# Kernel optimization log

Measured on AMD Instinct MI355X. Metric: run time of the kernel, lower is better.

## Reference

```python
import jax, jax.numpy as jnp
import numpy as np

N_NODES = 50000
N_EDGES = 800000
N_GRAPHS = 2500
HIDDEN = 64
IN_DIM = 14  # 11 QM9 features + 3 pos


def setup_inputs() -> dict:
    key = jax.random.key(0)
    ks = jax.random.split(key, 12)
    def glorot(k, shape):
        fan_in = shape[0]
        return jax.random.normal(k, shape, dtype=jnp.float32) / np.sqrt(fan_in)
    return {
        "x": jax.random.normal(ks[0], (N_NODES, 11), dtype=jnp.float32),
        "pos": jax.random.normal(ks[1], (N_NODES, 3), dtype=jnp.float32),
        "edge_index": jax.random.randint(ks[2], (2, N_EDGES), 0, N_NODES, dtype=jnp.int64),
        "batch": jnp.sort(jax.random.randint(ks[3], (N_NODES,), 0, N_GRAPHS, dtype=jnp.int64)),
        "W1a": glorot(ks[4], (IN_DIM, HIDDEN)),
        "b1a": jnp.zeros((HIDDEN,), jnp.float32),
        "W1b": glorot(ks[5], (HIDDEN, HIDDEN)),
        "b1b": jnp.zeros((HIDDEN,), jnp.float32),
        "W2a": glorot(ks[6], (HIDDEN, HIDDEN)),
        "b2a": jnp.zeros((HIDDEN,), jnp.float32),
        "W2b": glorot(ks[7], (HIDDEN, HIDDEN)),
        "b2b": jnp.zeros((HIDDEN,), jnp.float32),
        "Wlin": glorot(ks[8], (HIDDEN, 1)),
        "blin": jnp.zeros((1,), jnp.float32),
    }


def reference(x, pos, edge_index, batch, W1a, b1a, W1b, b1b, W2a, b2a, W2b, b2b, Wlin, blin):
    n = x.shape[0]
    src, dst = edge_index[0], edge_index[1]

    def gin_conv(h, Wa, ba, Wb, bb):
        # GINConv (eps=0): nn((1+eps)*h + sum_{j in N(i)} h_j)
        agg = jax.ops.segment_sum(h[src], dst, num_segments=n)  # scatter-add over edges
        z = h + agg
        return jax.nn.relu(z @ Wa + ba) @ Wb + bb

    h = jnp.concatenate([x, pos], axis=1)  # [N, 14]
    h = jax.nn.relu(gin_conv(h, W1a, b1a, W1b, b1b))
    h = jax.nn.relu(gin_conv(h, W2a, b2a, W2b, b2b))

    # global_mean_pool over graph ids
    sums = jax.ops.segment_sum(h, batch, num_segments=N_GRAPHS)            # [G, H]
    counts = jax.ops.segment_sum(jnp.ones((n,), h.dtype), batch, num_segments=N_GRAPHS)
    pooled = sums / jnp.maximum(counts, 1.0)[:, None]
    return pooled @ Wlin + blin  # [G, 1]
```

## Files before the change

kernel.cpp:

```cpp
#include <hip/hip_runtime.h>
#include <hip/hip_fp16.h>


typedef unsigned int uint;
typedef _Float16 half8 __attribute__((ext_vector_type(8)));
typedef float f32x4 __attribute__((ext_vector_type(4)));

#define BSH   6
#define NBKMAX 1024
#define EPB   4096
#define CAPSH 11
#define CAP   (1 << CAPSH)
#define ZBLK  64

__device__ __forceinline__ void addu(float* a, uint d) {
    __half2 h = *(__half2*)&d;
    a[0] += __low2float(h);
    a[1] += __high2float(h);
}
__device__ __forceinline__ half8 as_half8(uint4 u) {
    union { uint4 u; half8 h; } x; x.u = u; return x.h;
}


__global__ __launch_bounds__(256) void pack_bin(
    const float* __restrict__ x, const float* __restrict__ pos,
    uint2* __restrict__ xp2,
    const int* __restrict__ src, const int* __restrict__ dst,
    int* __restrict__ bkt_cnt, uint* __restrict__ pairs,
    const float* __restrict__ W1a, const float* __restrict__ W1b,
    const float* __restrict__ W2a, const float* __restrict__ W2b,
    _Float16* __restrict__ wp1a, _Float16* __restrict__ wp1b,
    _Float16* __restrict__ wp2a, _Float16* __restrict__ wp2b,
    uint4* __restrict__ zbuf, int nz4,
    int packb, int nbk, int N, int E)
{
    int bx = (int)blockIdx.x;
    if (bx < ZBLK) {
        uint4 z4 = {0u, 0u, 0u, 0u};
        for (int idx = bx * 256 + threadIdx.x; idx < nz4; idx += ZBLK * 256)
            zbuf[idx] = z4;
        return;
    }
    bx -= ZBLK;
    if (bx == 0) {
        for (int idx = threadIdx.x; idx < 64 * 32; idx += 256) {
            int n = idx >> 5, k = idx & 31;
            wp1a[idx] = (k < 14) ? (_Float16)W1a[k * 64 + n] : (_Float16)0.f;
        }
        for (int idx = threadIdx.x; idx < 64 * 64; idx += 256) {
            int n = idx >> 6, k = idx & 63;
            wp1b[idx] = (_Float16)W1b[k * 64 + n];
            wp2a[idx] = (_Float16)W2a[k * 64 + n];
            wp2b[idx] = (_Float16)W2b[k * 64 + n];
        }
        return;
    }
    bx -= 1;
    if (bx < packb) {
        int i = bx * 256 + threadIdx.x;
        if (i >= N) return;
        float v[16];
#pragma unroll
        for (int k = 0; k < 11; k++) v[k] = x[(size_t)i * 11 + k];
        v[11] = pos[(size_t)i * 3 + 0];
        v[12] = pos[(size_t)i * 3 + 1];
        v[13] = pos[(size_t)i * 3 + 2];
        v[14] = 0.f; v[15] = 0.f;
#pragma unroll
        for (int c = 0; c < 4; c++) {
            __half2 l = __floats2half2_rn(v[4 * c],     v[4 * c + 1]);
            __half2 h = __floats2half2_rn(v[4 * c + 2], v[4 * c + 3]);
            uint2 u;
            u.x = *(uint*)&l;
            u.y = *(uint*)&h;
            xp2[(size_t)i * 4 + c] = u;
        }
        return;
    }
    bx -= packb;
    __shared__ int lcnt[NBKMAX];
    __shared__ int lbase[NBKMAX];
    int tid = threadIdx.x;
    for (int i = tid; i < nbk; i += 256) lcnt[i] = 0;
    __syncthreads();
    int eb = bx * EPB;
    uint pv[16];
    int  rk[16], bk[16];
    if (eb + EPB <= E) {
        const int4* s4 = (const int4*)(src + eb) + tid * 4;
        const int4* d4 = (const int4*)(dst + eb) + tid * 4;
        int4 sv[4], dv[4];
#pragma unroll
        for (int g = 0; g < 4; g++) { sv[g] = s4[g]; dv[g] = d4[g]; }
#pragma unroll
        for (int g = 0; g < 4; g++) {
            int ss[4] = {sv[g].x, sv[g].y, sv[g].z, sv[g].w};
            int dd[4] = {dv[g].x, dv[g].y, dv[g].z, dv[g].w};
#pragma unroll
            for (int k = 0; k < 4; k++) {
                int j = g * 4 + k;
                bk[j] = dd[k] >> BSH;
                pv[j] = ((uint)(dd[k] & ((1 << BSH) - 1)) << 16) | (uint)ss[k];
            }
        }
#pragma unroll
        for (int j = 0; j < 16; j++)
            rk[j] = atomicAdd(&lcnt[bk[j]], 1);
    } else {
#pragma unroll
        for (int j = 0; j < 16; j++) {
            int e = eb + tid * 16 + j;
            bk[j] = -1;
            if (e < E) {
                int s = src[e];
                int d = dst[e];
                bk[j] = d >> BSH;
                pv[j] = ((uint)(d & ((1 << BSH) - 1)) << 16) | (uint)s;
            }
        }
#pragma unroll
        for (int j = 0; j < 16; j++)
            if (bk[j] >= 0) rk[j] = atomicAdd(&lcnt[bk[j]], 1);
    }
    __syncthreads();
    for (int i = tid; i < nbk; i += 256) {
        int c = lcnt[i];
        lbase[i] = c ? atomicAdd(&bkt_cnt[i], c) : 0;
    }
    __syncthreads();
#pragma unroll
    for (int j = 0; j < 16; j++) {
        if (bk[j] >= 0) {
            int p = lbase[bk[j]] + rk[j];
            if (p < CAP)
                pairs[((size_t)bk[j] << CAPSH) + p] = pv[j];
        }
    }
}


__global__ __launch_bounds__(256) void bucket_build(
    const uint* __restrict__ pairs, const int* __restrict__ bkt_cnt,
    int* __restrict__ offs, int* __restrict__ deg,
    int* __restrict__ ssrc, int N)
{
    __shared__ int cnt[64];
    __shared__ int cur[64];
    int b = blockIdx.x;
    int nbase = b << BSH;
    int nn = min(1 << BSH, N - nbase);
    int tid = threadIdx.x;
    if (tid < 64) cnt[tid] = 0;
    __syncthreads();
    int start = b << CAPSH;
    int cntE = min(bkt_cnt[b], CAP);
    uint pr[8];
#pragma unroll
    for (int k = 0; k < 8; k++) {
        int e = tid + k * 256;
        pr[k] = (e < cntE) ? pairs[start + e] : 0xffffffffu;
    }
#pragma unroll
    for (int k = 0; k < 8; k++)
        if (pr[k] != 0xffffffffu) atomicAdd(&cnt[pr[k] >> 16], 1);
    __syncthreads();
    if (tid < 64) {
        int v = cnt[tid];
        int s = v;
#pragma unroll
        for (int o2 = 1; o2 < 64; o2 <<= 1) {
            int t = __shfl_up(s, o2, 64);
            if (tid >= o2) s += t;
        }
        int gofs = start + s - v;
        if (tid < nn) {
            offs[nbase + tid] = gofs;
            deg[nbase + tid]  = v;
        }
        cur[tid] = gofs;
    }
    __syncthreads();
#pragma unroll
    for (int k = 0; k < 8; k++)
        if (pr[k] != 0xffffffffu) {
            int p = atomicAdd(&cur[pr[k] >> 16], 1);
            ssrc[p] = (int)(pr[k] & 0xffffu);
        }
}


__global__ __launch_bounds__(256) void gather1_mlp1(
    const uint2* __restrict__ xp2,
    const int* __restrict__ offs, const int* __restrict__ deg,
    const int* __restrict__ ssrc,
    const _Float16* __restrict__ wp1a, const _Float16* __restrict__ wp1b,
    const float* __restrict__ b1a, const float* __restrict__ b1b,
    uint* __restrict__ h1p)
{
    __shared__ uint4 zb[16 * 2];
    __shared__ float hb[16 * 68];
    int lane = threadIdx.x & 63;
    int wid  = threadIdx.x >> 6;
    int i0 = blockIdx.x << 4;
    int n0 = i0 + wid * 4;

    int stv = 0, lnv = 0;
    if (lane < 4) { stv = offs[n0 + lane]; lnv = deg[n0 + lane]; }
    int n  = lane >> 4;
    int s  = (lane >> 2) & 3;
    int c  = lane & 3;
    int dn = __shfl(lnv, n, 64);
    int st = __shfl(stv, n, 64);
    int pA = lane & 15;
    int svA = 0, svB = 0;
    if (dn > 0)  svA = ssrc[st + min(pA, dn - 1)];
    if (dn > 16) svB = ssrc[st + min(16 + pA, dn - 1)];
    uint2 S = {0u, 0u};
    if (s == 0) S = xp2[(size_t)(n0 + n) * 4 + c];

    float a[4] = {0.f, 0.f, 0.f, 0.f};
#pragma unroll
    for (int it = 0; it < 4; ++it) {
        int pos = it * 4 + s;
        int sA = __shfl(svA, (n << 4) | pos, 64);
        if (pos < dn) {
            uint2 A = xp2[(size_t)sA * 4 + c];
            addu(a + 0, A.x); addu(a + 2, A.y);
        }
    }
    if (__any(dn > 16)) {
#pragma unroll
        for (int it = 4; it < 8; ++it) {
            int pos = it * 4 + s;
            int sB = __shfl(svB, (n << 4) | (pos - 16), 64);
            if (pos < dn) {
                uint2 A = xp2[(size_t)sB * 4 + c];
                addu(a + 0, A.x); addu(a + 2, A.y);
            }
        }
        int pos2 = 32 + s;
        while (__any(pos2 < dn)) {
            if (pos2 < dn) {
                int sid = ssrc[st + pos2];
                uint2 A = xp2[(size_t)sid * 4 + c];
                addu(a + 0, A.x); addu(a + 2, A.y);
            }
            pos2 += 4;
        }
    }
#pragma unroll
    for (int mm = 4; mm <= 8; mm <<= 1)
#pragma unroll
        for (int d = 0; d < 4; d++) a[d] += __shfl_xor(a[d], mm, 64);
    if (s == 0) {
        addu(a + 0, S.x); addu(a + 2, S.y);
        __half2 l  = __floats2half2_rn(a[0], a[1]);
        __half2 hh = __floats2half2_rn(a[2], a[3]);
        uint2 u;
        u.x = *(uint*)&l;
        u.y = *(uint*)&hh;
        ((uint2*)zb)[(wid * 4 + n) * 4 + c] = u;
    }
    __syncthreads();

    int m = lane & 15, quad = lane >> 4;
    int half = lane >> 5, p = lane & 31;
    int nw = wid * 16 + m;
    half8 BA  = *(const half8*)(wp1a + (size_t)nw * 32 + quad * 8);
    half8 BB0 = *(const half8*)(wp1b + (size_t)nw * 64 + quad * 8);
    half8 BB1 = *(const half8*)(wp1b + (size_t)nw * 64 + 32 + quad * 8);
    float baw = b1a[nw], bbw = b1b[nw];

    half8 A0;
#pragma unroll
    for (int jj = 0; jj < 8; jj++) A0[jj] = (_Float16)0.f;
    if (quad < 2)
        A0 = as_half8(zb[m * 2 + quad]);
    f32x4 acc = (f32x4){baw, baw, baw, baw};
    acc = __builtin_amdgcn_mfma_f32_16x16x32_f16(A0, BA, acc, 0, 0, 0);
#pragma unroll
    for (int r = 0; r < 4; r++)
        hb[(quad * 4 + r) * 68 + wid * 16 + m] = fmaxf(acc[r], 0.f);
    __syncthreads();
    half8 A1[2];
#pragma unroll
    for (int hh = 0; hh < 2; hh++)
#pragma unroll
        for (int jj = 0; jj < 8; jj++)
            A1[hh][jj] = (_Float16)hb[m * 68 + hh * 32 + quad * 8 + jj];
    f32x4 acc2 = (f32x4){bbw, bbw, bbw, bbw};
    acc2 = __builtin_amdgcn_mfma_f32_16x16x32_f16(A1[0], BB0, acc2, 0, 0, 0);
    acc2 = __builtin_amdgcn_mfma_f32_16x16x32_f16(A1[1], BB1, acc2, 0, 0, 0);
    __syncthreads();
#pragma unroll
    for (int r = 0; r < 4; r++)
        hb[(quad * 4 + r) * 68 + wid * 16 + m] = fmaxf(acc2[r], 0.f);
    __syncthreads();
#pragma unroll
    for (int it = 0; it < 2; it++) {
        int row = wid * 4 + it * 2 + half;
        float lo = hb[row * 68 + 2 * p];
        float hi = hb[row * 68 + 2 * p + 1];
        __half2 hh2 = __floats2half2_rn(lo, hi);
        h1p[(size_t)(i0 + row) * 32 + p] = *(uint*)&hh2;
    }
}


__global__ __launch_bounds__(256) void gather2_mlp2pool(
    const uint4* __restrict__ h4,
    const int* __restrict__ offs, const int* __restrict__ deg,
    const int* __restrict__ ssrc,
    const _Float16* __restrict__ wp2a, const _Float16* __restrict__ wp2b,
    const float* __restrict__ b2a, const float* __restrict__ b2b,
    const int* __restrict__ batch,
    float* __restrict__ sums, float* __restrict__ counts)
{
    __shared__ uint4 zb[16 * 8];
    __shared__ float hb[16 * 68];
    int lane = threadIdx.x & 63;
    int wid  = threadIdx.x >> 6;
    int i0 = blockIdx.x << 4;
    int n0 = i0 + wid * 4;

    int stv = 0, lnv = 0;
    if (lane < 4) { stv = offs[n0 + lane]; lnv = deg[n0 + lane]; }
    int n  = lane >> 4;
    int s  = (lane >> 3) & 1;
    int q  = lane & 7;
    int dn = __shfl(lnv, n, 64);
    int st = __shfl(stv, n, 64);
    int pA = lane & 15;
    int svA = 0, svB = 0;
    if (dn > 0)  svA = ssrc[st + min(pA, dn - 1)];
    if (dn > 16) svB = ssrc[st + min(16 + pA, dn - 1)];
    uint4 S = {0u, 0u, 0u, 0u};
    if (s == 0) S = h4[(size_t)(n0 + n) * 8 + q];

    float a[8] = {0.f, 0.f, 0.f, 0.f, 0.f, 0.f, 0.f, 0.f};
#pragma unroll
    for (int it = 0; it < 8; ++it) {
        int pos = it * 2 + s;
        int sA = __shfl(svA, (n << 4) | pos, 64);
        if (pos < dn) {
            uint4 A = h4[(size_t)sA * 8 + q];
            addu(a + 0, A.x); addu(a + 2, A.y); addu(a + 4, A.z); addu(a + 6, A.w);
        }
    }
    if (__any(dn > 16)) {
#pragma unroll
        for (int it = 8; it < 16; ++it) {
            int pos = it * 2 + s;
            int sB = __shfl(svB, (n << 4) | (pos - 16), 64);
            if (pos < dn) {
                uint4 A = h4[(size_t)sB * 8 + q];
                addu(a + 0, A.x); addu(a + 2, A.y); addu(a + 4, A.z); addu(a + 6, A.w);
            }
        }
        int pos2 = 32 + s;
        while (__any(pos2 < dn)) {
            if (pos2 < dn) {
                int sid = ssrc[st + pos2];
                uint4 A = h4[(size_t)sid * 8 + q];
                addu(a + 0, A.x); addu(a + 2, A.y); addu(a + 4, A.z); addu(a + 6, A.w);
            }
            pos2 += 2;
        }
    }
#pragma unroll
    for (int d = 0; d < 8; d++) a[d] += __shfl_xor(a[d], 8, 64);
    if (s == 0) {
        addu(a + 0, S.x); addu(a + 2, S.y); addu(a + 4, S.z); addu(a + 6, S.w);
        __half2 p0 = __floats2half2_rn(a[0], a[1]);
        __half2 p1 = __floats2half2_rn(a[2], a[3]);
        __half2 p2 = __floats2half2_rn(a[4], a[5]);
        __half2 p3 = __floats2half2_rn(a[6], a[7]);
        uint4 o4;
        o4.x = *(uint*)&p0; o4.y = *(uint*)&p1;
        o4.z = *(uint*)&p2; o4.w = *(uint*)&p3;
        zb[(wid * 4 + n) * 8 + q] = o4;
    }
    __syncthreads();

    int m = lane & 15, quad = lane >> 4;
    int nw = wid * 16 + m;
    half8 BA0 = *(const half8*)(wp2a + (size_t)nw * 64 + quad * 8);
    half8 BA1 = *(const half8*)(wp2a + (size_t)nw * 64 + 32 + quad * 8);
    half8 BB0 = *(const half8*)(wp2b + (size_t)nw * 64 + quad * 8);
    half8 BB1 = *(const half8*)(wp2b + (size_t)nw * 64 + 32 + quad * 8);
    float baw = b2a[nw], bbw = b2b[nw];

    half8 A0[2];
#pragma unroll
    for (int hh = 0; hh < 2; hh++)
        A0[hh] = as_half8(zb[m * 8 + hh * 4 + quad]);
    f32x4 acc = (f32x4){baw, baw, baw, baw};
    acc = __builtin_amdgcn_mfma_f32_16x16x32_f16(A0[0], BA0, acc, 0, 0, 0);
    acc = __builtin_amdgcn_mfma_f32_16x16x32_f16(A0[1], BA1, acc, 0, 0, 0);
#pragma unroll
    for (int r = 0; r < 4; r++)
        hb[(quad * 4 + r) * 68 + wid * 16 + m] = fmaxf(acc[r], 0.f);
    __syncthreads();
    half8 A1[2];
#pragma unroll
    for (int hh = 0; hh < 2; hh++)
#pragma unroll
        for (int jj = 0; jj < 8; jj++)
            A1[hh][jj] = (_Float16)hb[m * 68 + hh * 32 + quad * 8 + jj];
    f32x4 acc2 = (f32x4){bbw, bbw, bbw, bbw};
    acc2 = __builtin_amdgcn_mfma_f32_16x16x32_f16(A1[0], BB0, acc2, 0, 0, 0);
    acc2 = __builtin_amdgcn_mfma_f32_16x16x32_f16(A1[1], BB1, acc2, 0, 0, 0);
    __syncthreads();
#pragma unroll
    for (int r = 0; r < 4; r++)
        hb[(quad * 4 + r) * 68 + wid * 16 + m] = fmaxf(acc2[r], 0.f);
    __syncthreads();

    int gcur = batch[i0 + wid * 4]; float ps = 0.f; int cntn = 0;
#pragma unroll
    for (int nn = 0; nn < 4; nn++) {
        int row = wid * 4 + nn;
        float v = hb[row * 68 + lane];
        int gi = batch[i0 + row];
        if (gi != gcur) {
            atomicAdd(&sums[gcur * 64 + lane], ps);
            if (lane == 0) atomicAdd(&counts[gcur], (float)cntn);
            gcur = gi; ps = 0.f; cntn = 0;
        }
        ps += v; cntn++;
    }
    atomicAdd(&sums[gcur * 64 + lane], ps);
    if (lane == 0) atomicAdd(&counts[gcur], (float)cntn);
}

__global__ __launch_bounds__(256) void gin_final(
    const float* __restrict__ sums, const float* __restrict__ counts,
    const float* __restrict__ Wlin, const float* __restrict__ blin,
    float* __restrict__ out, int G)
{
    int lane = threadIdx.x & 63;
    int g    = blockIdx.x * 4 + (threadIdx.x >> 6);
    if (g < G) {
        float v = sums[g * 64 + lane] * Wlin[lane];
#pragma unroll
        for (int off = 32; off > 0; off >>= 1) v += __shfl_down(v, off, 64);
        if (lane == 0) out[g] = v / fmaxf(counts[g], 1.0f) + blin[0];
    }
}

extern "C" void kernel_launch(void* const* d_in, const int* in_sizes, int n_in,
                              void* d_out, int out_size, void* d_ws, size_t ws_size,
                              hipStream_t stream) {
    const float* x    = (const float*)d_in[0];
    const float* pos  = (const float*)d_in[1];
    const int*   ei   = (const int*)d_in[2];
    const int*   batch= (const int*)d_in[3];
    const float* W1a  = (const float*)d_in[4];
    const float* b1a  = (const float*)d_in[5];
    const float* W1b  = (const float*)d_in[6];
    const float* b1b  = (const float*)d_in[7];
    const float* W2a  = (const float*)d_in[8];
    const float* b2a  = (const float*)d_in[9];
    const float* W2b  = (const float*)d_in[10];
    const float* b2b  = (const float*)d_in[11];
    const float* Wlin = (const float*)d_in[12];
    const float* blin = (const float*)d_in[13];
    float* out = (float*)d_out;

    const int N = in_sizes[0] / 11;
    const int E = in_sizes[2] / 2;
    const int G = out_size;

    const int* src = ei;
    const int* dst = ei + E;
    const int nbk   = (N + (1 << BSH) - 1) >> BSH;
    const int packb = (N + 255) / 256;
    const int neb   = (E + EPB - 1) / EPB;
    const int NG    = N >> 4;

    char* ws = (char*)d_ws;
    size_t o = 0;
    float* sums    = (float*)(ws + o); o += (size_t)G * 64 * 4;
    float* counts  = (float*)(ws + o); o += (((size_t)G + 63) & ~(size_t)63) * 4;
    const int nz4  = (int)(((size_t)G * 64 + (((size_t)G + 63) & ~(size_t)63)) / 4);
    int*   bkt_cnt = (int*)(ws + o);   o += NBKMAX * 4;
    o = (o + 255) & ~(size_t)255;
    _Float16* wp1a = (_Float16*)(ws + o); o += 64 * 32 * 2;
    o = (o + 255) & ~(size_t)255;
    _Float16* wp1b = (_Float16*)(ws + o); o += 64 * 64 * 2;
    o = (o + 255) & ~(size_t)255;
    _Float16* wp2a = (_Float16*)(ws + o); o += 64 * 64 * 2;
    o = (o + 255) & ~(size_t)255;
    _Float16* wp2b = (_Float16*)(ws + o); o += 64 * 64 * 2;
    o = (o + 255) & ~(size_t)255;
    int*   offs    = (int*)(ws + o);   o += (size_t)N * 4;
    int*   deg     = (int*)(ws + o);   o += (size_t)N * 4;
    o = (o + 255) & ~(size_t)255;
    int*   ssrc    = (int*)(ws + o);   o += ((size_t)nbk << CAPSH) * 4;
    o = (o + 255) & ~(size_t)255;
    uint*  h1p     = (uint*)(ws + o);  o += (size_t)N * 32 * 4;
    o = (o + 255) & ~(size_t)255;
    uint2* xp2     = (uint2*)(ws + o); o += (size_t)N * 32;
    o = (o + 255) & ~(size_t)255;
    uint*  pairs   = (uint*)(ws + o);  o += ((size_t)nbk << CAPSH) * 4;

    hipMemsetAsync(bkt_cnt, 0, NBKMAX * 4, stream);

    pack_bin<<<ZBLK + 1 + packb + neb, 256, 0, stream>>>(
        x, pos, xp2, src, dst, bkt_cnt, pairs,
        W1a, W1b, W2a, W2b, wp1a, wp1b, wp2a, wp2b,
        (uint4*)sums, nz4, packb, nbk, N, E);
    bucket_build<<<nbk, 256, 0, stream>>>(pairs, bkt_cnt, offs, deg, ssrc, N);
    gather1_mlp1<<<NG, 256, 0, stream>>>(
        xp2, offs, deg, ssrc, wp1a, wp1b, b1a, b1b, h1p);
    gather2_mlp2pool<<<NG, 256, 0, stream>>>(
        (const uint4*)h1p, offs, deg, ssrc, wp2a, wp2b, b2a, b2b,
        batch, sums, counts);
    gin_final<<<(G + 3) / 4, 256, 0, stream>>>(
        sums, counts, Wlin, blin, out, G);
}
```

Measured before the change: 148.3 us.

## Make gather+MLP kernels persistent with grid-stride loop and prefetched offsets

Both gather/MLP kernels now launch at most 1536 blocks and loop over 16-node groups in a grid-stride fashion, instead of one block per group. While the current group finishes, the offsets and degrees for the next group are prefetched. A second shared buffer (hb2) removes one __syncthreads per iteration. This aims to cut block launch and teardown overhead and hide index-load latency. The risk is less latency hiding across blocks and load imbalance across the persistent blocks.

```diff
diff --git a/kernel.cpp b/kernel.cpp
--- a/kernel.cpp
+++ b/kernel.cpp
@@ -12,6 +12,7 @@
 #define CAPSH 11
 #define CAP   (1 << CAPSH)
 #define ZBLK  64
+#define PERS  1536
 
 __device__ __forceinline__ void addu(float* a, uint d) {
     __half2 h = *(__half2*)&d;
@@ -196,114 +197,127 @@
     const int* __restrict__ ssrc,
     const _Float16* __restrict__ wp1a, const _Float16* __restrict__ wp1b,
     const float* __restrict__ b1a, const float* __restrict__ b1b,
-    uint* __restrict__ h1p)
+    uint* __restrict__ h1p, int NG, int nblk)
 {
     __shared__ uint4 zb[16 * 2];
     __shared__ float hb[16 * 68];
+    __shared__ float hb2[16 * 68];
     int lane = threadIdx.x & 63;
     int wid  = threadIdx.x >> 6;
-    int i0 = blockIdx.x << 4;
-    int n0 = i0 + wid * 4;
-
-    int stv = 0, lnv = 0;
-    if (lane < 4) { stv = offs[n0 + lane]; lnv = deg[n0 + lane]; }
     int n  = lane >> 4;
     int s  = (lane >> 2) & 3;
     int c  = lane & 3;
-    int dn = __shfl(lnv, n, 64);
-    int st = __shfl(stv, n, 64);
     int pA = lane & 15;
-    int svA = 0, svB = 0;
-    if (dn > 0)  svA = ssrc[st + min(pA, dn - 1)];
-    if (dn > 16) svB = ssrc[st + min(16 + pA, dn - 1)];
-    uint2 S = {0u, 0u};
-    if (s == 0) S = xp2[(size_t)(n0 + n) * 4 + c];
-
-    float a[4] = {0.f, 0.f, 0.f, 0.f};
-#pragma unroll
-    for (int it = 0; it < 4; ++it) {
-        int pos = it * 4 + s;
-        int sA = __shfl(svA, (n << 4) | pos, 64);
-        if (pos < dn) {
-            uint2 A = xp2[(size_t)sA * 4 + c];
-            addu(a + 0, A.x); addu(a + 2, A.y);
-        }
-    }
-    if (__any(dn > 16)) {
-#pragma unroll
-        for (int it = 4; it < 8; ++it) {
+    int m = lane & 15, quad = lane >> 4;
+    int half_ = lane >> 5, p = lane & 31;
+    int nw = wid * 16 + m;
+
+    int g = blockIdx.x;
+    if (g >= NG) return;
+    int stv = 0, lnv = 0;
+    if (lane < 4) {
+        int n0 = (g << 4) + wid * 4;
+        stv = offs[n0 + lane]; lnv = deg[n0 + lane];
+    }
+    for (; g < NG; g += nblk) {
+        int i0 = g << 4;
+        int n0 = i0 + wid * 4;
+        int dn = __shfl(lnv, n, 64);
+        int st = __shfl(stv, n, 64);
+        int svA = 0, svB = 0;
+        if (dn > 0)  svA = ssrc[st + min(pA, dn - 1)];
+        if (dn > 16) svB = ssrc[st + min(16 + pA, dn - 1)];
+        uint2 S = {0u, 0u};
+        if (s == 0) S = xp2[(size_t)(n0 + n) * 4 + c];
+        float a[4] = {0.f, 0.f, 0.f, 0.f};
+#pragma unroll
+        for (int it = 0; it < 4; ++it) {
             int pos = it * 4 + s;
-            int sB = __shfl(svB, (n << 4) | (pos - 16), 64);
+            int sA = __shfl(svA, (n << 4) | pos, 64);
             if (pos < dn) {
-                uint2 A = xp2[(size_t)sB * 4 + c];
+                uint2 A = xp2[(size_t)sA * 4 + c];
                 addu(a + 0, A.x); addu(a + 2, A.y);
             }
         }
-        int pos2 = 32 + s;
-        while (__any(pos2 < dn)) {
-            if (pos2 < dn) {
-                int sid = ssrc[st + pos2];
-                uint2 A = xp2[(size_t)sid * 4 + c];
-                addu(a + 0, A.x); addu(a + 2, A.y);
-            }
-            pos2 += 4;
-        }
-    }
-#pragma unroll
-    for (int mm = 4; mm <= 8; mm <<= 1)
-#pragma unroll
-        for (int d = 0; d < 4; d++) a[d] += __shfl_xor(a[d], mm, 64);
-    if (s == 0) {
-        addu(a + 0, S.x); addu(a + 2, S.y);
-        __half2 l  = __floats2half2_rn(a[0], a[1]);
-        __half2 hh = __floats2half2_rn(a[2], a[3]);
-        uint2 u;
-        u.x = *(uint*)&l;
-        u.y = *(uint*)&hh;
-        ((uint2*)zb)[(wid * 4 + n) * 4 + c] = u;
-    }
-    __syncthreads();
-
-    int m = lane & 15, quad = lane >> 4;
-    int half = lane >> 5, p = lane & 31;
-    int nw = wid * 16 + m;
-    half8 BA  = *(const half8*)(wp1a + (size_t)nw * 32 + quad * 8);
-    half8 BB0 = *(const half8*)(wp1b + (size_t)nw * 64 + quad * 8);
-    half8 BB1 = *(const half8*)(wp1b + (size_t)nw * 64 + 32 + quad * 8);
-    float baw = b1a[nw], bbw = b1b[nw];
-
-    half8 A0;
-#pragma unroll
-    for (int jj = 0; jj < 8; jj++) A0[jj] = (_Float16)0.f;
-    if (quad < 2)
-        A0 = as_half8(zb[m * 2 + quad]);
-    f32x4 acc = (f32x4){baw, baw, baw, baw};
-    acc = __builtin_amdgcn_mfma_f32_16x16x32_f16(A0, BA, acc, 0, 0, 0);
-#pragma unroll
-    for (int r = 0; r < 4; r++)
-        hb[(quad * 4 + r) * 68 + wid * 16 + m] = fmaxf(acc[r], 0.f);
-    __syncthreads();
-    half8 A1[2];
-#pragma unroll
-    for (int hh = 0; hh < 2; hh++)
-#pragma unroll
-        for (int jj = 0; jj < 8; jj++)
-            A1[hh][jj] = (_Float16)hb[m * 68 + hh * 32 + quad * 8 + jj];
-    f32x4 acc2 = (f32x4){bbw, bbw, bbw, bbw};
-    acc2 = __builtin_amdgcn_mfma_f32_16x16x32_f16(A1[0], BB0, acc2, 0, 0, 0);
-    acc2 = __builtin_amdgcn_mfma_f32_16x16x32_f16(A1[1], BB1, acc2, 0, 0, 0);
-    __syncthreads();
-#pragma unroll
-    for (int r = 0; r < 4; r++)
-        hb[(quad * 4 + r) * 68 + wid * 16 + m] = fmaxf(acc2[r], 0.f);
-    __syncthreads();
-#pragma unroll
-    for (int it = 0; it < 2; it++) {
-        int row = wid * 4 + it * 2 + half;
-        float lo = hb[row * 68 + 2 * p];
-        float hi = hb[row * 68 + 2 * p + 1];
-        __half2 hh2 = __floats2half2_rn(lo, hi);
-        h1p[(size_t)(i0 + row) * 32 + p] = *(uint*)&hh2;
+        if (__any(dn > 16)) {
+#pragma unroll
+            for (int it = 4; it < 8; ++it) {
+                int pos = it * 4 + s;
+                int sB = __shfl(svB, (n << 4) | (pos - 16), 64);
+                if (pos < dn) {
+                    uint2 A = xp2[(size_t)sB * 4 + c];
+                    addu(a + 0, A.x); addu(a + 2, A.y);
+                }
+            }
+            int pos2 = 32 + s;
+            while (__any(pos2 < dn)) {
+                if (pos2 < dn) {
+                    int sid = ssrc[st + pos2];
+                    uint2 A = xp2[(size_t)sid * 4 + c];
+                    addu(a + 0, A.x); addu(a + 2, A.y);
+                }
+                pos2 += 4;
+            }
+        }
+#pragma unroll
+        for (int mm = 4; mm <= 8; mm <<= 1)
+#pragma unroll
+            for (int d = 0; d < 4; d++) a[d] += __shfl_xor(a[d], mm, 64);
+        if (s == 0) {
+            addu(a + 0, S.x); addu(a + 2, S.y);
+            __half2 l  = __floats2half2_rn(a[0], a[1]);
+            __half2 hh = __floats2half2_rn(a[2], a[3]);
+            uint2 u;
+            u.x = *(uint*)&l;
+            u.y = *(uint*)&hh;
+            ((uint2*)zb)[(wid * 4 + n) * 4 + c] = u;
+        }
+        {
+            int gn = g + nblk;
+            if (gn < NG && lane < 4) {
+                int n0n = (gn << 4) + wid * 4;
+                stv = offs[n0n + lane]; lnv = deg[n0n + lane];
+            }
+        }
+        __syncthreads();
+
+        half8 BA  = *(const half8*)(wp1a + (size_t)nw * 32 + quad * 8);
+        float baw = b1a[nw];
+        half8 A0;
+#pragma unroll
+        for (int jj = 0; jj < 8; jj++) A0[jj] = (_Float16)0.f;
+        if (quad < 2)
+            A0 = as_half8(zb[m * 2 + quad]);
+        f32x4 acc = (f32x4){baw, baw, baw, baw};
+        acc = __builtin_amdgcn_mfma_f32_16x16x32_f16(A0, BA, acc, 0, 0, 0);
+#pragma unroll
+        for (int r = 0; r < 4; r++)
+            hb[(quad * 4 + r) * 68 + wid * 16 + m] = fmaxf(acc[r], 0.f);
+        __syncthreads();
+        half8 BB0 = *(const half8*)(wp1b + (size_t)nw * 64 + quad * 8);
+        half8 BB1 = *(const half8*)(wp1b + (size_t)nw * 64 + 32 + quad * 8);
+        float bbw = b1b[nw];
+        half8 A1[2];
+#pragma unroll
+        for (int hh = 0; hh < 2; hh++)
+#pragma unroll
+            for (int jj = 0; jj < 8; jj++)
+                A1[hh][jj] = (_Float16)hb[m * 68 + hh * 32 + quad * 8 + jj];
+        f32x4 acc2 = (f32x4){bbw, bbw, bbw, bbw};
+        acc2 = __builtin_amdgcn_mfma_f32_16x16x32_f16(A1[0], BB0, acc2, 0, 0, 0);
+        acc2 = __builtin_amdgcn_mfma_f32_16x16x32_f16(A1[1], BB1, acc2, 0, 0, 0);
+#pragma unroll
+        for (int r = 0; r < 4; r++)
+            hb2[(quad * 4 + r) * 68 + wid * 16 + m] = fmaxf(acc2[r], 0.f);
+        __syncthreads();
+#pragma unroll
+        for (int it = 0; it < 2; it++) {
+            int row = wid * 4 + it * 2 + half_;
+            float lo = hb2[row * 68 + 2 * p];
+            float hi = hb2[row * 68 + 2 * p + 1];
+            __half2 hh2 = __floats2half2_rn(lo, hi);
+            h1p[(size_t)(i0 + row) * 32 + p] = *(uint*)&hh2;
+        }
     }
 }
 
@@ -315,123 +329,136 @@
     const _Float16* __restrict__ wp2a, const _Float16* __restrict__ wp2b,
     const float* __restrict__ b2a, const float* __restrict__ b2b,
     const int* __restrict__ batch,
-    float* __restrict__ sums, float* __restrict__ counts)
+    float* __restrict__ sums, float* __restrict__ counts, int NG, int nblk)
 {
     __shared__ uint4 zb[16 * 8];
     __shared__ float hb[16 * 68];
+    __shared__ float hb2[16 * 68];
     int lane = threadIdx.x & 63;
     int wid  = threadIdx.x >> 6;
-    int i0 = blockIdx.x << 4;
-    int n0 = i0 + wid * 4;
-
-    int stv = 0, lnv = 0;
-    if (lane < 4) { stv = offs[n0 + lane]; lnv = deg[n0 + lane]; }
     int n  = lane >> 4;
     int s  = (lane >> 3) & 1;
     int q  = lane & 7;
-    int dn = __shfl(lnv, n, 64);
-    int st = __shfl(stv, n, 64);
     int pA = lane & 15;
-    int svA = 0, svB = 0;
-    if (dn > 0)  svA = ssrc[st + min(pA, dn - 1)];
-    if (dn > 16) svB = ssrc[st + min(16 + pA, dn - 1)];
-    uint4 S = {0u, 0u, 0u, 0u};
-    if (s == 0) S = h4[(size_t)(n0 + n) * 8 + q];
-
-    float a[8] = {0.f, 0.f, 0.f, 0.f, 0.f, 0.f, 0.f, 0.f};
-#pragma unroll
-    for (int it = 0; it < 8; ++it) {
-        int pos = it * 2 + s;
-        int sA = __shfl(svA, (n << 4) | pos, 64);
-        if (pos < dn) {
-            uint4 A = h4[(size_t)sA * 8 + q];
-            addu(a + 0, A.x); addu(a + 2, A.y); addu(a + 4, A.z); addu(a + 6, A.w);
-        }
-    }
-    if (__any(dn > 16)) {
-#pragma unroll
-        for (int it = 8; it < 16; ++it) {
-            int pos = it * 2 + s;
-            int sB = __shfl(svB, (n << 4) | (pos - 16), 64);
-            if (pos < dn) {
-                uint4 A = h4[(size_t)sB * 8 + q];
-                addu(a + 0, A.x); addu(a + 2, A.y); addu(a + 4, A.z); addu(a + 6, A.w);
-            }
-        }
-        int pos2 = 32 + s;
-        while (__any(pos2 < dn)) {
-            if (pos2 < dn) {
-                int sid = ssrc[st + pos2];
-                uint4 A = h4[(size_t)sid * 8 + q];
-                addu(a + 0, A.x); addu(a + 2, A.y); addu(a + 4, A.z); addu(a + 6, A.w);
-            }
-            pos2 += 2;
-        }
-    }
-#pragma unroll
-    for (int d = 0; d < 8; d++) a[d] += __shfl_xor(a[d], 8, 64);
-    if (s == 0) {
-        addu(a + 0, S.x); addu(a + 2, S.y); addu(a + 4, S.z); addu(a + 6, S.w);
-        __half2 p0 = __floats2half2_rn(a[0], a[1]);
-        __half2 p1 = __floats2half2_rn(a[2], a[3]);
-        __half2 p2 = __floats2half2_rn(a[4], a[5]);
-        __half2 p3 = __floats2half2_rn(a[6], a[7]);
-        uint4 o4;
-        o4.x = *(uint*)&p0; o4.y = *(uint*)&p1;
-        o4.z = *(uint*)&p2; o4.w = *(uint*)&p3;
-        zb[(wid * 4 + n) * 8 + q] = o4;
-    }
-    __syncthreads();
-
     int m = lane & 15, quad = lane >> 4;
     int nw = wid * 16 + m;
-    half8 BA0 = *(const half8*)(wp2a + (size_t)nw * 64 + quad * 8);
-    half8 BA1 = *(const half8*)(wp2a + (size_t)nw * 64 + 32 + quad * 8);
-    half8 BB0 = *(const half8*)(wp2b + (size_t)nw * 64 + quad * 8);
-    half8 BB1 = *(const half8*)(wp2b + (size_t)nw * 64 + 32 + quad * 8);
-    float baw = b2a[nw], bbw = b2b[nw];
-
-    half8 A0[2];
-#pragma unroll
-    for (int hh = 0; hh < 2; hh++)
-        A0[hh] = as_half8(zb[m * 8 + hh * 4 + quad]);
-    f32x4 acc = (f32x4){baw, baw, baw, baw};
-    acc = __builtin_amdgcn_mfma_f32_16x16x32_f16(A0[0], BA0, acc, 0, 0, 0);
-    acc = __builtin_amdgcn_mfma_f32_16x16x32_f16(A0[1], BA1, acc, 0, 0, 0);
-#pragma unroll
-    for (int r = 0; r < 4; r++)
-        hb[(quad * 4 + r) * 68 + wid * 16 + m] = fmaxf(acc[r], 0.f);
-    __syncthreads();
-    half8 A1[2];
-#pragma unroll
-    for (int hh = 0; hh < 2; hh++)
-#pragma unroll
-        for (int jj = 0; jj < 8; jj++)
-            A1[hh][jj] = (_Float16)hb[m * 68 + hh * 32 + quad * 8 + jj];
-    f32x4 acc2 = (f32x4){bbw, bbw, bbw, bbw};
-    acc2 = __builtin_amdgcn_mfma_f32_16x16x32_f16(A1[0], BB0, acc2, 0, 0, 0);
-    acc2 = __builtin_amdgcn_mfma_f32_16x16x32_f16(A1[1], BB1, acc2, 0, 0, 0);
-    __syncthreads();
-#pragma unroll
-    for (int r = 0; r < 4; r++)
-        hb[(quad * 4 + r) * 68 + wid * 16 + m] = fmaxf(acc2[r], 0.f);
-    __syncthreads();
-
-    int gcur = batch[i0 + wid * 4]; float ps = 0.f; int cntn = 0;
-#pragma unroll
-    for (int nn = 0; nn < 4; nn++) {
-        int row = wid * 4 + nn;
-        float v = hb[row * 68 + lane];
-        int gi = batch[i0 + row];
-        if (gi != gcur) {
-            atomicAdd(&sums[gcur * 64 + lane], ps);
-            if (lane == 0) atomicAdd(&counts[gcur], (float)cntn);
-            gcur = gi; ps = 0.f; cntn = 0;
-        }
-        ps += v; cntn++;
-    }
-    atomicAdd(&sums[gcur * 64 + lane], ps);
-    if (lane == 0) atomicAdd(&counts[gcur], (float)cntn);
+
+    int g = blockIdx.x;
+    if (g >= NG) return;
+    int stv = 0, lnv = 0;
+    if (lane < 4) {
+        int n0 = (g << 4) + wid * 4;
+        stv = offs[n0 + lane]; lnv = deg[n0 + lane];
+    }
+    for (; g < NG; g += nblk) {
+        int i0 = g << 4;
+        int n0 = i0 + wid * 4;
+        int dn = __shfl(lnv, n, 64);
+        int st = __shfl(stv, n, 64);
+        int svA = 0, svB = 0;
+        if (dn > 0)  svA = ssrc[st + min(pA, dn - 1)];
+        if (dn > 16) svB = ssrc[st + min(16 + pA, dn - 1)];
+        uint4 S = {0u, 0u, 0u, 0u};
+        if (s == 0) S = h4[(size_t)(n0 + n) * 8 + q];
+        float a[8] = {0.f, 0.f, 0.f, 0.f, 0.f, 0.f, 0.f, 0.f};
+#pragma unroll
+        for (int it = 0; it < 8; ++it) {
+            int pos = it * 2 + s;
+            int sA = __shfl(svA, (n << 4) | pos, 64);
+            if (pos < dn) {
+                uint4 A = h4[(size_t)sA * 8 + q];
+                addu(a + 0, A.x); addu(a + 2, A.y); addu(a + 4, A.z); addu(a + 6, A.w);
+            }
+        }
+        if (__any(dn > 16)) {
+#pragma unroll
+            for (int it = 8; it < 16; ++it) {
+                int pos = it * 2 + s;
+                int sB = __shfl(svB, (n << 4) | (pos - 16), 64);
+                if (pos < dn) {
+                    uint4 A = h4[(size_t)sB * 8 + q];
+                    addu(a + 0, A.x); addu(a + 2, A.y); addu(a + 4, A.z); addu(a + 6, A.w);
+                }
+            }
+            int pos2 = 32 + s;
+            while (__any(pos2 < dn)) {
+                if (pos2 < dn) {
+                    int sid = ssrc[st + pos2];
+                    uint4 A = h4[(size_t)sid * 8 + q];
+                    addu(a + 0, A.x); addu(a + 2, A.y); addu(a + 4, A.z); addu(a + 6, A.w);
+                }
+                pos2 += 2;
+            }
+        }
+#pragma unroll
+        for (int d = 0; d < 8; d++) a[d] += __shfl_xor(a[d], 8, 64);
+        if (s == 0) {
+            addu(a + 0, S.x); addu(a + 2, S.y); addu(a + 4, S.z); addu(a + 6, S.w);
+            __half2 p0 = __floats2half2_rn(a[0], a[1]);
+            __half2 p1 = __floats2half2_rn(a[2], a[3]);
+            __half2 p2 = __floats2half2_rn(a[4], a[5]);
+            __half2 p3 = __floats2half2_rn(a[6], a[7]);
+            uint4 o4;
+            o4.x = *(uint*)&p0; o4.y = *(uint*)&p1;
+            o4.z = *(uint*)&p2; o4.w = *(uint*)&p3;
+            zb[(wid * 4 + n) * 8 + q] = o4;
+        }
+        {
+            int gn = g + nblk;
+            if (gn < NG && lane < 4) {
+                int n0n = (gn << 4) + wid * 4;
+                stv = offs[n0n + lane]; lnv = deg[n0n + lane];
+            }
+        }
+        __syncthreads();
+
+        half8 BA0 = *(const half8*)(wp2a + (size_t)nw * 64 + quad * 8);
+        half8 BA1 = *(const half8*)(wp2a + (size_t)nw * 64 + 32 + quad * 8);
+        float baw = b2a[nw];
+        half8 A0[2];
+#pragma unroll
+        for (int hh = 0; hh < 2; hh++)
+            A0[hh] = as_half8(zb[m * 8 + hh * 4 + quad]);
+        f32x4 acc = (f32x4){baw, baw, baw, baw};
+        acc = __builtin_amdgcn_mfma_f32_16x16x32_f16(A0[0], BA0, acc, 0, 0, 0);
+        acc = __builtin_amdgcn_mfma_f32_16x16x32_f16(A0[1], BA1, acc, 0, 0, 0);
+#pragma unroll
+        for (int r = 0; r < 4; r++)
+            hb[(quad * 4 + r) * 68 + wid * 16 + m] = fmaxf(acc[r], 0.f);
+        __syncthreads();
+        half8 BB0 = *(const half8*)(wp2b + (size_t)nw * 64 + quad * 8);
+        half8 BB1 = *(const half8*)(wp2b + (size_t)nw * 64 + 32 + quad * 8);
+        float bbw = b2b[nw];
+        half8 A1[2];
+#pragma unroll
+        for (int hh = 0; hh < 2; hh++)
+#pragma unroll
+            for (int jj = 0; jj < 8; jj++)
+                A1[hh][jj] = (_Float16)hb[m * 68 + hh * 32 + quad * 8 + jj];
+        f32x4 acc2 = (f32x4){bbw, bbw, bbw, bbw};
+        acc2 = __builtin_amdgcn_mfma_f32_16x16x32_f16(A1[0], BB0, acc2, 0, 0, 0);
+        acc2 = __builtin_amdgcn_mfma_f32_16x16x32_f16(A1[1], BB1, acc2, 0, 0, 0);
+#pragma unroll
+        for (int r = 0; r < 4; r++)
+            hb2[(quad * 4 + r) * 68 + wid * 16 + m] = fmaxf(acc2[r], 0.f);
+        __syncthreads();
+
+        int gcur = batch[i0 + wid * 4]; float ps = 0.f; int cntn = 0;
+#pragma unroll
+        for (int nn = 0; nn < 4; nn++) {
+            int row = wid * 4 + nn;
+            float v = hb2[row * 68 + lane];
+            int gi = batch[i0 + row];
+            if (gi != gcur) {
+                atomicAdd(&sums[gcur * 64 + lane], ps);
+                if (lane == 0) atomicAdd(&counts[gcur], (float)cntn);
+                gcur = gi; ps = 0.f; cntn = 0;
+            }
+            ps += v; cntn++;
+        }
+        atomicAdd(&sums[gcur * 64 + lane], ps);
+        if (lane == 0) atomicAdd(&counts[gcur], (float)cntn);
+    }
 }
 
 __global__ __launch_bounds__(256) void gin_final(
@@ -478,6 +505,7 @@
     const int packb = (N + 255) / 256;
     const int neb   = (E + EPB - 1) / EPB;
     const int NG    = N >> 4;
+    const int gblk  = (NG < PERS) ? NG : PERS;
 
     char* ws = (char*)d_ws;
     size_t o = 0;
@@ -512,11 +540,11 @@
         W1a, W1b, W2a, W2b, wp1a, wp1b, wp2a, wp2b,
         (uint4*)sums, nz4, packb, nbk, N, E);
     bucket_build<<<nbk, 256, 0, stream>>>(pairs, bkt_cnt, offs, deg, ssrc, N);
-    gather1_mlp1<<<NG, 256, 0, stream>>>(
-        xp2, offs, deg, ssrc, wp1a, wp1b, b1a, b1b, h1p);
-    gather2_mlp2pool<<<NG, 256, 0, stream>>>(
+    gather1_mlp1<<<gblk, 256, 0, stream>>>(
+        xp2, offs, deg, ssrc, wp1a, wp1b, b1a, b1b, h1p, NG, gblk);
+    gather2_mlp2pool<<<gblk, 256, 0, stream>>>(
         (const uint4*)h1p, offs, deg, ssrc, wp2a, wp2b, b2a, b2b,
-        batch, sums, counts);
+        batch, sums, counts, NG, gblk);
     gin_final<<<(G + 3) / 4, 256, 0, stream>>>(
         sums, counts, Wlin, blin, out, G);
 }
```

New measurement: 153.8 us. 1.04x slower.
